# Performance work log

Hardware: AMD Instinct MI355X
Metric: run time of the kernel (lower is better)

## Reference

```python
import jax, jax.numpy as jnp
import numpy as np

NEG_SLOPE = 0.2  # PyG GATConv default leaky_relu slope
EPS = 1e-16     # PyG softmax denominator epsilon


def gat_conv(x, src, dst, edge_attr, W, att_src, att_dst, W_edge, att_edge, bias):
    """Single-head PyG GATConv with edge_dim. x:[N,Fin] -> [N,Fout].
    src/dst already include self-loops; edge_attr matches their length."""
    N = x.shape[0]
    h = x @ W                      # [N, Fout] transformed node features
    a_s = h @ att_src              # [N] per-node source logit contribution
    a_d = h @ att_dst              # [N]
    a_e = (edge_attr @ W_edge) @ att_edge   # [E] edge contribution
    logits = jax.nn.leaky_relu(a_s[src] + a_d[dst] + a_e, NEG_SLOPE)  # [E]
    # segment softmax over destination nodes
    m = jax.ops.segment_max(logits, dst, num_segments=N)    # [N]
    m = jnp.where(jnp.isfinite(m), m, 0.0)
    e = jnp.exp(logits - m[dst])                             # [E]
    denom = jax.ops.segment_sum(e, dst, num_segments=N)      # [N]
    alpha = e / (denom[dst] + EPS)                            # [E]
    # scatter-aggregate weighted messages
    out = jax.ops.segment_sum(alpha[:, None] * h[src], dst, num_segments=N)
    return out + bias


def setup_inputs() -> dict:
    key = jax.random.key(0)
    ks = jax.random.split(key, 16)
    N, E, F_in, H, C, ED = 100000, 1600000, 128, 64, 2, 1
    inp = {
        "x": jax.random.normal(ks[0], (N, F_in), dtype=jnp.float32),
        "edge_index": jax.random.randint(ks[1], (2, E), 0, N, dtype=jnp.int32),
        "edge_attr": jax.random.normal(ks[2], (E, ED), dtype=jnp.float32),
        # layer 1 params (Glorot-ish scale)
        "W1": jax.random.normal(ks[3], (F_in, H), dtype=jnp.float32) * (1.0 / np.sqrt(F_in)),
        "att_src1": jax.random.normal(ks[4], (H,), dtype=jnp.float32) * (1.0 / np.sqrt(H)),
        "att_dst1": jax.random.normal(ks[5], (H,), dtype=jnp.float32) * (1.0 / np.sqrt(H)),
        "W_edge1": jax.random.normal(ks[6], (ED, H), dtype=jnp.float32),
        "att_edge1": jax.random.normal(ks[7], (H,), dtype=jnp.float32) * (1.0 / np.sqrt(H)),
        "bias1": jnp.zeros((H,), dtype=jnp.float32),
        # layer 2 params
        "W2": jax.random.normal(ks[8], (H, C), dtype=jnp.float32) * (1.0 / np.sqrt(H)),
        "att_src2": jax.random.normal(ks[9], (C,), dtype=jnp.float32),
        "att_dst2": jax.random.normal(ks[10], (C,), dtype=jnp.float32),
        "W_edge2": jax.random.normal(ks[11], (ED, C), dtype=jnp.float32),
        "att_edge2": jax.random.normal(ks[12], (C,), dtype=jnp.float32),
        "bias2": jnp.zeros((C,), dtype=jnp.float32),
    }
    return inp


def reference(x, edge_index, edge_attr,
              W1, att_src1, att_dst1, W_edge1, att_edge1, bias1,
              W2, att_src2, att_dst2, W_edge2, att_edge2, bias2):
    N = x.shape[0]
    # PyG GATConv add_self_loops=True, fill_value='mean' for edge_attr
    loop = jnp.arange(N, dtype=edge_index.dtype)
    src = jnp.concatenate([edge_index[0], loop])
    dst = jnp.concatenate([edge_index[1], loop])
    ea_mean = jnp.mean(edge_attr, axis=0, keepdims=True)              # [1, ED]
    ea = jnp.concatenate([edge_attr, jnp.broadcast_to(ea_mean, (N, edge_attr.shape[1]))])

    h = gat_conv(x, src, dst, ea, W1, att_src1, att_dst1, W_edge1, att_edge1, bias1)
    h = jax.nn.relu(h)  # dropout is identity in eval mode
    out = gat_conv(h, src, dst, ea, W2, att_src2, att_dst2, W_edge2, att_edge2, bias2)
    return jax.nn.log_softmax(out, axis=1)
```

## Files before the change

### kernel.cpp

```cpp
#include <hip/hip_runtime.h>
#include <math.h>

#define NEG_SLOPE 0.2f
#define EPSF 1e-16f

constexpr int FIN = 128;
constexpr int H   = 64;
constexpr int C   = 2;
constexpr int BSHIFT = 8;
constexpr int NBUCK_MAX = 1024;
constexpr int CHUNK = 4096;
constexpr int CAP   = 6144;

typedef short v8s __attribute__((ext_vector_type(8)));
typedef float v4f __attribute__((ext_vector_type(4)));
typedef unsigned short u16;

__device__ inline void split_bf16(float v, u16& hi, u16& lo) {
    unsigned u = __float_as_uint(v);
    unsigned r = (u + 0x7FFFu + ((u >> 16) & 1u)) >> 16;
    hi = (u16)r;
    float hf = __uint_as_float(r << 16);
    float l = v - hf;
    unsigned ul = __float_as_uint(l);
    lo = (u16)((ul + 0x7FFFu + ((ul >> 16) & 1u)) >> 16);
}

__device__ inline u16 to_bf16(float v) {
    unsigned u = __float_as_uint(v);
    return (u16)((u + 0x7FFFu + ((u >> 16) & 1u)) >> 16);
}
__device__ inline float blo(int v) { return __uint_as_float((unsigned)v << 16); }
__device__ inline float bhi(int v) { return __uint_as_float((unsigned)v & 0xFFFF0000u); }

__device__ inline int scan1024_excl(int v, int* wtot, int t) {
    int lane = t & 63, w = t >> 6;
    int incl = v;
    #pragma unroll
    for (int o = 1; o < 64; o <<= 1) {
        int u = __shfl_up(incl, o, 64);
        if (lane >= o) incl += u;
    }
    if (lane == 63) wtot[w] = incl;
    __syncthreads();
    int woff = 0;
    for (int i = 0; i < w; i++) woff += wtot[i];
    return woff + incl - v;
}

__global__ __launch_bounds__(1024) void pre_kernel(const float* __restrict__ ea,
                                                   const int* __restrict__ dst, int E,
                                                   float* __restrict__ csum, int* __restrict__ cnt,
                                                   const float* __restrict__ W1,
                                                   u16* __restrict__ Wt_hi, u16* __restrict__ Wt_lo,
                                                   int NBUCK) {
    int c = blockIdx.x, t = threadIdx.x;
    int gid = c * 1024 + t;
    if (gid < FIN * H) {
        int k = gid >> 6, f = gid & 63;
        u16 h, l;
        split_bf16(W1[gid], h, l);
        int idx = ((k >> 3) << 9) + (f << 3) + (k & 7);
        Wt_hi[idx] = h;
        Wt_lo[idx] = l;
    }
    __shared__ int lh[NBUCK_MAX];
    __shared__ float wsum[16];
    lh[t] = 0;
    __syncthreads();
    int base = c * CHUNK;
    int cntE = min(CHUNK, E - base);
    float acc = 0.f;
    for (int i = t; i < cntE; i += 1024) {
        int e = base + i;
        acc += ea[e];
        atomicAdd(&lh[dst[e] >> BSHIFT], 1);
    }
    for (int off = 32; off; off >>= 1) acc += __shfl_down(acc, off, 64);
    int lane = t & 63, wv = t >> 6;
    if (lane == 0) wsum[wv] = acc;
    __syncthreads();
    if (t == 0) {
        float s = 0.f;
        #pragma unroll
        for (int i = 0; i < 16; i++) s += wsum[i];
        csum[c] = s;
    }
    if (t < NBUCK) cnt[(size_t)c * NBUCK + t] = lh[t];
}

__global__ __launch_bounds__(256) void soff_kernel(const int* __restrict__ cnt,
                                                   int NBUCK, int NCHUNK,
                                                   int* __restrict__ bcount, int* __restrict__ poff,
                                                   const float* __restrict__ csum, int E,
                                                   const float* __restrict__ W_edge1,
                                                   const float* __restrict__ att_edge1,
                                                   const float* __restrict__ W_edge2,
                                                   const float* __restrict__ att_edge2,
                                                   float* __restrict__ scal,
                                                   int* __restrict__ rowN) {
    int b = blockIdx.x, t = threadIdx.x;
    int per = (NCHUNK + 255) / 256;
    int v[8];
    int s = 0;
    for (int j = 0; j < per; j++) {
        int c = t * per + j;
        v[j] = (c < NCHUNK) ? cnt[(size_t)c * NBUCK + b] : 0;
        s += v[j];
    }
    __shared__ int red[256];
    __shared__ float ws4[4];
    red[t] = s;
    __syncthreads();
    for (int off = 1; off < 256; off <<= 1) {
        int u = (t >= off) ? red[t - off] : 0;
        __syncthreads();
        red[t] += u;
        __syncthreads();
    }
    int run = red[t] - s;
    for (int j = 0; j < per; j++) {
        int c = t * per + j;
        if (c < NCHUNK) poff[(size_t)b * NCHUNK + c] = run;
        run += v[j];
    }
    if (t == 255) bcount[b] = red[255];
    if (b == 0) {
        float acc = 0.f;
        for (int i = t; i < NCHUNK; i += 256) acc += csum[i];
        for (int off = 32; off; off >>= 1) acc += __shfl_down(acc, off, 64);
        if ((t & 63) == 0) ws4[t >> 6] = acc;
        __syncthreads();
        if (t == 0) {
            float tot = ws4[0] + ws4[1] + ws4[2] + ws4[3];
            float c1 = 0.f;
            for (int i = 0; i < H; i++) c1 += W_edge1[i] * att_edge1[i];
            float c2 = 0.f;
            for (int i = 0; i < C; i++) c2 += W_edge2[i] * att_edge2[i];
            scal[0] = tot / (float)E; scal[1] = c1; scal[2] = c2;
            *rowN = E;
        }
    }
}

__global__ __launch_bounds__(1024) void stage_kernel(
        const int* __restrict__ src, const int* __restrict__ dst, const float* __restrict__ ea,
        int E, const int* __restrict__ cnt, const int* __restrict__ poff,
        const int* __restrict__ bcount,
        int2* __restrict__ staging, int* __restrict__ bbase_out, int NBUCK, int NCHUNK) {
    __shared__ int   bb[NBUCK_MAX];
    __shared__ int   cur[NBUCK_MAX];
    __shared__ int   gofs[NBUCK_MAX];
    __shared__ int2  sbuf[CHUNK];
    __shared__ short sbkt[CHUNK];
    __shared__ int   wt16[16];
    int t = threadIdx.x;
    int c = blockIdx.x;
    int base = c * CHUNK;
    int cntE = min(CHUNK, E - base);
    int bv = (t < NBUCK) ? bcount[t] : 0;
    int bx = scan1024_excl(bv, wt16, t);
    if (t < NBUCK) bb[t] = bx;
    if (c == 0) {
        if (t < NBUCK) bbase_out[t] = bx;
        if (t == 0) bbase_out[NBUCK] = E;
    }
    __syncthreads();
    int h = (t < NBUCK) ? cnt[(size_t)c * NBUCK + t] : 0;
    int p = scan1024_excl(h, wt16, t);
    if (t < NBUCK) {
        if (h) gofs[t] = bb[t] + poff[(size_t)t * NCHUNK + c] - p;
        cur[t] = p;
    }
    __syncthreads();
    for (int i = t; i < cntE; i += 1024) {
        int e = base + i;
        int d = dst[e];
        int b = d >> BSHIFT;
        int slot = atomicAdd(&cur[b], 1);
        sbuf[slot] = make_int2(src[e] | ((d & ((1 << BSHIFT) - 1)) << 20), __float_as_int(ea[e]));
        sbkt[slot] = (short)b;
    }
    __syncthreads();
    for (int j = t; j < cntE; j += 1024)
        staging[gofs[sbkt[j]] + j] = sbuf[j];
}

__global__ __launch_bounds__(256) void gemm1_mfma_kernel(
        const float* __restrict__ x,
        const u16* __restrict__ Wt_hi, const u16* __restrict__ Wt_lo,
        const float* __restrict__ att_src, const float* __restrict__ att_dst,
        u16* __restrict__ h1b, float* __restrict__ a_s, float* __restrict__ a_d, int N) {
    __shared__ u16 WhL[FIN * H];
    __shared__ u16 WlL[FIN * H];
    int t = threadIdx.x;
    int w = t >> 6, lane = t & 63;
    int m = lane & 15, q = lane >> 4;
    int base = blockIdx.x * 128 + w * 32;
    int n0 = base + m;
    int n1 = base + 16 + m;
    bool in0 = n0 < N, in1 = n1 < N;
    const float* xr0 = x + (size_t)n0 * FIN;
    const float* xr1 = x + (size_t)n1 * FIN;

    float4 fh[4], fl4[4];
    {
        const float4* gh = (const float4*)Wt_hi;
        const float4* gl = (const float4*)Wt_lo;
        #pragma unroll
        for (int i = 0; i < 4; i++) {
            fh[i]  = gh[t + i * 256];
            fl4[i] = gl[t + i * 256];
        }
    }
    float4 xa[8], xb[8];
    #pragma unroll
    for (int kt = 0; kt < 4; kt++) {
        if (in0) {
            const float4* p = (const float4*)(xr0 + kt * 32 + q * 8);
            xa[kt * 2] = p[0]; xa[kt * 2 + 1] = p[1];
        } else {
            xa[kt * 2] = make_float4(0.f, 0.f, 0.f, 0.f);
            xa[kt * 2 + 1] = make_float4(0.f, 0.f, 0.f, 0.f);
        }
        if (in1) {
            const float4* p = (const float4*)(xr1 + kt * 32 + q * 8);
            xb[kt * 2] = p[0]; xb[kt * 2 + 1] = p[1];
        } else {
            xb[kt * 2] = make_float4(0.f, 0.f, 0.f, 0.f);
            xb[kt * 2 + 1] = make_float4(0.f, 0.f, 0.f, 0.f);
        }
    }
    {
        float4* sh = (float4*)WhL;
        float4* sl = (float4*)WlL;
        #pragma unroll
        for (int i = 0; i < 4; i++) {
            sh[t + i * 256] = fh[i];
            sl[t + i * 256] = fl4[i];
        }
    }

    v8s ah0[4], al0[4], ah1[4], al1[4];
    #pragma unroll
    for (int kt = 0; kt < 4; kt++) {
        float va[8], vb[8];
        va[0] = xa[kt*2].x; va[1] = xa[kt*2].y; va[2] = xa[kt*2].z; va[3] = xa[kt*2].w;
        va[4] = xa[kt*2+1].x; va[5] = xa[kt*2+1].y; va[6] = xa[kt*2+1].z; va[7] = xa[kt*2+1].w;
        vb[0] = xb[kt*2].x; vb[1] = xb[kt*2].y; vb[2] = xb[kt*2].z; vb[3] = xb[kt*2].w;
        vb[4] = xb[kt*2+1].x; vb[5] = xb[kt*2+1].y; vb[6] = xb[kt*2+1].z; vb[7] = xb[kt*2+1].w;
        #pragma unroll
        for (int j = 0; j < 8; j++) {
            u16 hb, lb;
            split_bf16(va[j], hb, lb);
            ah0[kt][j] = (short)hb; al0[kt][j] = (short)lb;
            split_bf16(vb[j], hb, lb);
            ah1[kt][j] = (short)hb; al1[kt][j] = (short)lb;
        }
    }
    __syncthreads();

    float ps0[4] = {0,0,0,0}, pd0[4] = {0,0,0,0};
    float ps1[4] = {0,0,0,0}, pd1[4] = {0,0,0,0};
    #pragma unroll
    for (int ft = 0; ft < 4; ft++) {
        v4f acc0 = {0.f, 0.f, 0.f, 0.f};
        v4f acc1 = {0.f, 0.f, 0.f, 0.f};
        #pragma unroll
        for (int kt = 0; kt < 4; kt++) {
            int fi = ((kt * 4 + q) << 9) + ((ft * 16 + m) << 3);
            v8s bh = *(const v8s*)(WhL + fi);
            v8s bl = *(const v8s*)(WlL + fi);
            acc0 = __builtin_amdgcn_mfma_f32_16x16x32_bf16(ah0[kt], bh, acc0, 0, 0, 0);
            acc0 = __builtin_amdgcn_mfma_f32_16x16x32_bf16(al0[kt], bh, acc0, 0, 0, 0);
            acc0 = __builtin_amdgcn_mfma_f32_16x16x32_bf16(ah0[kt], bl, acc0, 0, 0, 0);
            acc1 = __builtin_amdgcn_mfma_f32_16x16x32_bf16(ah1[kt], bh, acc1, 0, 0, 0);
            acc1 = __builtin_amdgcn_mfma_f32_16x16x32_bf16(al1[kt], bh, acc1, 0, 0, 0);
            acc1 = __builtin_amdgcn_mfma_f32_16x16x32_bf16(ah1[kt], bl, acc1, 0, 0, 0);
        }
        int f = ft * 16 + m;
        float asf = att_src[f], adf = att_dst[f];
        #pragma unroll
        for (int r = 0; r < 4; r++) {
            int nd0 = base + q * 4 + r;
            int nd1 = base + 16 + q * 4 + r;
            if (nd0 < N) h1b[(size_t)nd0 * H + f] = to_bf16(acc0[r]);
            if (nd1 < N) h1b[(size_t)nd1 * H + f] = to_bf16(acc1[r]);
            ps0[r] += acc0[r] * asf; pd0[r] += acc0[r] * adf;
            ps1[r] += acc1[r] * asf; pd1[r] += acc1[r] * adf;
        }
    }
    #pragma unroll
    for (int msk = 1; msk < 16; msk <<= 1) {
        #pragma unroll
        for (int r = 0; r < 4; r++) {
            ps0[r] += __shfl_xor(ps0[r], msk, 64);
            pd0[r] += __shfl_xor(pd0[r], msk, 64);
            ps1[r] += __shfl_xor(ps1[r], msk, 64);
            pd1[r] += __shfl_xor(pd1[r], msk, 64);
        }
    }
    if (m == 0) {
        #pragma unroll
        for (int r = 0; r < 4; r++) {
            int nd0 = base + q * 4 + r;
            int nd1 = base + 16 + q * 4 + r;
            if (nd0 < N) { a_s[nd0] = ps0[r]; a_d[nd0] = pd0[r]; }
            if (nd1 < N) { a_s[nd1] = ps1[r]; a_d[nd1] = pd1[r]; }
        }
    }
}

__global__ __launch_bounds__(1024) void bfin_kernel(
        const int2* __restrict__ staging, const int* __restrict__ bbase,
        const float* __restrict__ scal,
        const float* __restrict__ a_s1, const float* __restrict__ a_d1,
        int* __restrict__ row, int2* __restrict__ sedge, float* __restrict__ sea2, int N) {
    __shared__ int   nh[256];
    __shared__ int   wt16[16];
    __shared__ int2  ebuf[CAP];
    __shared__ float abuf[CAP];
    int b = blockIdx.x, t = threadIdx.x;
    int beg = bbase[b], end = bbase[b + 1];
    int cnt = end - beg;
    int node0 = b << BSHIFT;
    float c1 = scal[1];
    if (t < 256) nh[t] = 0;
    __syncthreads();
    for (int i = beg + t; i < end; i += 1024)
        atomicAdd(&nh[(unsigned)staging[i].x >> 20], 1);
    __syncthreads();
    int v = (t < 256) ? nh[t] : 0;
    int lane = t & 63, w = t >> 6;
    int incl = v;
    #pragma unroll
    for (int o = 1; o < 64; o <<= 1) {
        int u = __shfl_up(incl, o, 64);
        if (lane >= o) incl += u;
    }
    if (w < 4 && lane == 63) wt16[w] = incl;
    __syncthreads();
    int woff = 0;
    int wl = w < 4 ? w : 4;
    for (int i = 0; i < wl; i++) woff += wt16[i];
    int excl = woff + incl - v;
    int node = node0 + t;
    if (t < 256 && node < N) row[node] = beg + excl;
    bool fast = (cnt <= CAP);
    if (t < 256) nh[t] = fast ? excl : beg + excl;
    __syncthreads();
    for (int i = beg + t; i < end; i += 1024) {
        int2 r = staging[i];
        int dlow = (unsigned)r.x >> 20;
        int sn = r.x & 0xFFFFF;
        float eav = __int_as_float(r.y);
        float lg = a_s1[sn] + a_d1[node0 + dlow] + eav * c1;
        lg = lg > 0.f ? lg : NEG_SLOPE * lg;
        float ex = __expf(lg);
        int pos = atomicAdd(&nh[dlow], 1);
        if (fast) {
            ebuf[pos] = make_int2(sn, __float_as_int(ex));
            abuf[pos] = eav;
        } else {
            sedge[pos] = make_int2(sn, __float_as_int(ex));
            sea2[pos] = eav;
        }
    }
    __syncthreads();
    if (fast) {
        for (int j = t; j < cnt; j += 1024) {
            sedge[beg + j] = ebuf[j];
            sea2[beg + j]  = abuf[j];
        }
    }
}

__device__ inline void accum8(float acc[8], float& den, float xw, int4 hv) {
    den += xw;
    acc[0] += xw * blo(hv.x); acc[1] += xw * bhi(hv.x);
    acc[2] += xw * blo(hv.y); acc[3] += xw * bhi(hv.y);
    acc[4] += xw * blo(hv.z); acc[5] += xw * bhi(hv.z);
    acc[6] += xw * blo(hv.w); acc[7] += xw * bhi(hv.w);
}

__global__ __launch_bounds__(256) void agg1_kernel(
        const int* __restrict__ row, const int2* __restrict__ sedge,
        const float* __restrict__ scal,
        const float* __restrict__ a_s, const float* __restrict__ a_d,
        const u16* __restrict__ h1b,
        const float* __restrict__ bias1, const float* __restrict__ W2,
        const float* __restrict__ att_src2, const float* __restrict__ att_dst2,
        float* __restrict__ h2, float* __restrict__ a_s2, float* __restrict__ a_d2,
        int N) {
    int wv = threadIdx.x >> 6;
    int lane = threadIdx.x & 63;
    int g  = lane >> 3;
    int fl = lane & 7;
    int n = blockIdx.x * 32 + wv * 8 + g;
    if (n >= N) return;
    int beg = row[n], end = row[n + 1];
    float den = 0.f;
    float acc[8] = {0.f, 0.f, 0.f, 0.f, 0.f, 0.f, 0.f, 0.f};
    const u16* hrow = h1b + fl * 8;
    int i = beg;
    for (; i + 8 <= end; i += 8) {
        int2 e[8]; int4 hv[8];
        #pragma unroll
        for (int j = 0; j < 8; j++) e[j] = sedge[i + j];
        #pragma unroll
        for (int j = 0; j < 8; j++) hv[j] = *(const int4*)(hrow + (size_t)e[j].x * H);
        #pragma unroll
        for (int j = 0; j < 8; j++) accum8(acc, den, __int_as_float(e[j].y), hv[j]);
    }
    if (i + 4 <= end) {
        int2 e0 = sedge[i], e1 = sedge[i + 1], e2 = sedge[i + 2], e3 = sedge[i + 3];
        int4 h0 = *(const int4*)(hrow + (size_t)e0.x * H);
        int4 h1v = *(const int4*)(hrow + (size_t)e1.x * H);
        int4 h2v = *(const int4*)(hrow + (size_t)e2.x * H);
        int4 h3v = *(const int4*)(hrow + (size_t)e3.x * H);
        accum8(acc, den, __int_as_float(e0.y), h0);
        accum8(acc, den, __int_as_float(e1.y), h1v);
        accum8(acc, den, __int_as_float(e2.y), h2v);
        accum8(acc, den, __int_as_float(e3.y), h3v);
        i += 4;
    }
    if (i + 2 <= end) {
        int2 e0 = sedge[i], e1 = sedge[i + 1];
        int4 h0 = *(const int4*)(hrow + (size_t)e0.x * H);
        int4 h1v = *(const int4*)(hrow + (size_t)e1.x * H);
        accum8(acc, den, __int_as_float(e0.y), h0);
        accum8(acc, den, __int_as_float(e1.y), h1v);
        i += 2;
    }
    if (i < end) {
        int2 e0 = sedge[i];
        int4 h0 = *(const int4*)(hrow + (size_t)e0.x * H);
        accum8(acc, den, __int_as_float(e0.y), h0);
    }
    {
        float lg = a_s[n] + a_d[n] + scal[0] * scal[1];
        lg = lg > 0.f ? lg : NEG_SLOPE * lg;
        float ex = __expf(lg);
        int4 hs = *(const int4*)(hrow + (size_t)n * H);
        accum8(acc, den, ex, hs);
    }
    float inv = 1.f / (den + EPSF);
    float p0 = 0.f, p1 = 0.f;
    #pragma unroll
    for (int k = 0; k < 8; k++) {
        int f = fl * 8 + k;
        float hr = acc[k] * inv + bias1[f];
        hr = fmaxf(hr, 0.f);
        p0 += hr * W2[f * C + 0];
        p1 += hr * W2[f * C + 1];
    }
    #pragma unroll
    for (int msk = 1; msk < 8; msk <<= 1) {
        p0 += __shfl_xor(p0, msk, 64);
        p1 += __shfl_xor(p1, msk, 64);
    }
    if (fl == 0) {
        h2[(size_t)n * C + 0] = p0;
        h2[(size_t)n * C + 1] = p1;
        a_s2[n] = p0 * att_src2[0] + p1 * att_src2[1];
        a_d2[n] = p0 * att_dst2[0] + p1 * att_dst2[1];
    }
}

__global__ __launch_bounds__(256) void agg2_kernel(
        const int* __restrict__ row, const int2* __restrict__ sedge, const float* __restrict__ sea2,
        const float* __restrict__ scal,
        const float* __restrict__ a_s2, const float* __restrict__ a_d2,
        const float* __restrict__ h2, const float* __restrict__ bias2,
        float* __restrict__ out, int N) {
    int wv = threadIdx.x >> 6;
    int lane = threadIdx.x & 63;
    int g  = lane >> 3;
    int fl = lane & 7;
    int n = blockIdx.x * 32 + wv * 8 + g;
    if (n >= N) return;
    float c2 = scal[2];
    float ad = a_d2[n];
    int beg = row[n], end = row[n + 1];
    float den = 0.f, m0 = 0.f, m1 = 0.f;
    for (int i = beg + fl; i < end; i += 8) {
        int s = sedge[i].x;
        float lg = a_s2[s] + ad + sea2[i] * c2;
        lg = lg > 0.f ? lg : NEG_SLOPE * lg;
        float ex = __expf(lg);
        den += ex;
        m0 += ex * h2[(size_t)s * C + 0];
        m1 += ex * h2[(size_t)s * C + 1];
    }
    if (fl == 0) {
        float lg = a_s2[n] + ad + scal[0] * c2;
        lg = lg > 0.f ? lg : NEG_SLOPE * lg;
        float ex = __expf(lg);
        den += ex;
        m0 += ex * h2[(size_t)n * C + 0];
        m1 += ex * h2[(size_t)n * C + 1];
    }
    #pragma unroll
    for (int msk = 1; msk < 8; msk <<= 1) {
        den += __shfl_xor(den, msk, 64);
        m0  += __shfl_xor(m0, msk, 64);
        m1  += __shfl_xor(m1, msk, 64);
    }
    if (fl == 0) {
        float dn = den + EPSF;
        float o0 = m0 / dn + bias2[0];
        float o1 = m1 / dn + bias2[1];
        float mx = fmaxf(o0, o1);
        float lse = mx + logf(expf(o0 - mx) + expf(o1 - mx));
        out[(size_t)n * C + 0] = o0 - lse;
        out[(size_t)n * C + 1] = o1 - lse;
    }
}

extern "C" void kernel_launch(void* const* d_in, const int* in_sizes, int n_in,
                              void* d_out, int out_size, void* d_ws, size_t ws_size,
                              hipStream_t stream) {
    const float* x        = (const float*)d_in[0];
    const int*   ei       = (const int*)d_in[1];
    const float* ea       = (const float*)d_in[2];
    const float* W1       = (const float*)d_in[3];
    const float* att_src1 = (const float*)d_in[4];
    const float* att_dst1 = (const float*)d_in[5];
    const float* W_edge1  = (const float*)d_in[6];
    const float* att_edge1= (const float*)d_in[7];
    const float* bias1    = (const float*)d_in[8];
    const float* W2       = (const float*)d_in[9];
    const float* att_src2 = (const float*)d_in[10];
    const float* att_dst2 = (const float*)d_in[11];
    const float* W_edge2  = (const float*)d_in[12];
    const float* att_edge2= (const float*)d_in[13];
    const float* bias2    = (const float*)d_in[14];

    const int N  = in_sizes[0] / FIN;
    const int E  = in_sizes[1] / 2;
    const int* srcp = ei;
    const int* dstp = ei + E;
    const int NBUCK  = (N + (1 << BSHIFT) - 1) >> BSHIFT;
    const int NCHUNK = (E + CHUNK - 1) / CHUNK;

    char* wsb = (char*)d_ws;
    size_t off = 0;
    auto alloc = [&](size_t bytes) { void* p = wsb + off; off += (bytes + 255) & ~size_t(255); return p; };
    float* csum   = (float*)alloc((size_t)2048 * 4);
    int*   bcount = (int*)alloc((size_t)NBUCK_MAX * 4);
    int*   bbase  = (int*)alloc((size_t)(NBUCK_MAX + 1) * 4);
    int*   cnt    = (int*)alloc((size_t)NCHUNK * NBUCK * 4);
    int*   poff   = (int*)alloc((size_t)NBUCK * NCHUNK * 4);
    int*   row    = (int*)alloc((size_t)(N + 1) * 4);
    int2*  sedge  = (int2*)alloc((size_t)(E + 8) * 8);
    float* sea2   = (float*)alloc((size_t)E * 4);
    int2*  staging= (int2*)alloc((size_t)E * 8);
    u16*   h1b    = (u16*)alloc((size_t)N * H * 2);
    u16*   Wt_hi  = (u16*)alloc((size_t)FIN * H * 2);
    u16*   Wt_lo  = (u16*)alloc((size_t)FIN * H * 2);
    float* a_s1   = (float*)alloc((size_t)N * 4);
    float* a_d1   = (float*)alloc((size_t)N * 4);
    float* h2     = (float*)alloc((size_t)N * C * 4);
    float* a_s2   = (float*)alloc((size_t)N * 4);
    float* a_d2   = (float*)alloc((size_t)N * 4);
    float* scal   = (float*)alloc(3 * 4);

    pre_kernel<<<NCHUNK, 1024, 0, stream>>>(ea, dstp, E, csum, cnt, W1, Wt_hi, Wt_lo, NBUCK);
    soff_kernel<<<NBUCK, 256, 0, stream>>>(cnt, NBUCK, NCHUNK, bcount, poff,
                                           csum, E, W_edge1, att_edge1, W_edge2, att_edge2,
                                           scal, row + N);
    stage_kernel<<<NCHUNK, 1024, 0, stream>>>(srcp, dstp, ea, E, cnt, poff, bcount,
                                              staging, bbase, NBUCK, NCHUNK);
    gemm1_mfma_kernel<<<(N + 127) / 128, 256, 0, stream>>>(x, Wt_hi, Wt_lo, att_src1, att_dst1,
                                                           h1b, a_s1, a_d1, N);
    bfin_kernel<<<NBUCK, 1024, 0, stream>>>(staging, bbase, scal, a_s1, a_d1, row, sedge, sea2, N);
    agg1_kernel<<<(N + 31) / 32, 256, 0, stream>>>(row, sedge, scal, a_s1, a_d1, h1b,
                                                   bias1, W2, att_src2, att_dst2,
                                                   h2, a_s2, a_d2, N);
    agg2_kernel<<<(N + 31) / 32, 256, 0, stream>>>(row, sedge, sea2, scal, a_s2, a_d2, h2, bias2,
                                                   (float*)d_out, N);
}
```

Baseline: 213.4 us.

## Fuse bucket finalize with layer-1 aggregation using LDS-resident edge lists

Merges bfin and agg1 into one kernel. Each 1024-thread block sorts its 256-node bucket's edges into LDS and aggregates layer-1 messages straight from there, so the sorted edge list is no longer written to and re-read from global memory for layer 1. The sea2 array is dropped by packing the edge attribute into the sedge payload, which agg2 now reads in a single int2 load. The cost is that only 1024 threads per block handle the 256 nodes' gathers, with no 8-way unrolling, and the large LDS footprint limits occupancy during the latency-bound gather phase.

```diff
diff --git a/kernel.cpp b/kernel.cpp
--- a/kernel.cpp
+++ b/kernel.cpp
@@ -311,12 +311,25 @@
     }
 }
 
-__global__ __launch_bounds__(1024) void bfin_kernel(
+__device__ inline void accum8(float acc[8], float& den, float xw, int4 hv) {
+    den += xw;
+    acc[0] += xw * blo(hv.x); acc[1] += xw * bhi(hv.x);
+    acc[2] += xw * blo(hv.y); acc[3] += xw * bhi(hv.y);
+    acc[4] += xw * blo(hv.z); acc[5] += xw * bhi(hv.z);
+    acc[6] += xw * blo(hv.w); acc[7] += xw * bhi(hv.w);
+}
+
+__global__ __launch_bounds__(1024) void bfin_agg1_kernel(
         const int2* __restrict__ staging, const int* __restrict__ bbase,
         const float* __restrict__ scal,
         const float* __restrict__ a_s1, const float* __restrict__ a_d1,
-        int* __restrict__ row, int2* __restrict__ sedge, float* __restrict__ sea2, int N) {
+        const u16* __restrict__ h1b,
+        const float* __restrict__ bias1, const float* __restrict__ W2,
+        const float* __restrict__ att_src2, const float* __restrict__ att_dst2,
+        int* __restrict__ row, int2* __restrict__ sedge,
+        float* __restrict__ h2, float* __restrict__ a_s2, float* __restrict__ a_d2, int N) {
     __shared__ int   nh[256];
+    __shared__ int   bg[256];
     __shared__ int   wt16[16];
     __shared__ int2  ebuf[CAP];
     __shared__ float abuf[CAP];
@@ -344,131 +357,108 @@
     int wl = w < 4 ? w : 4;
     for (int i = 0; i < wl; i++) woff += wt16[i];
     int excl = woff + incl - v;
-    int node = node0 + t;
-    if (t < 256 && node < N) row[node] = beg + excl;
+    if (t < 256 && node0 + t < N) row[node0 + t] = beg + excl;
     bool fast = (cnt <= CAP);
-    if (t < 256) nh[t] = fast ? excl : beg + excl;
+    if (t < 256) {
+        bg[t] = excl;
+        nh[t] = fast ? excl : beg + excl;
+    }
     __syncthreads();
     for (int i = beg + t; i < end; i += 1024) {
         int2 r = staging[i];
         int dlow = (unsigned)r.x >> 20;
         int sn = r.x & 0xFFFFF;
         float eav = __int_as_float(r.y);
-        float lg = a_s1[sn] + a_d1[node0 + dlow] + eav * c1;
-        lg = lg > 0.f ? lg : NEG_SLOPE * lg;
-        float ex = __expf(lg);
         int pos = atomicAdd(&nh[dlow], 1);
         if (fast) {
-            ebuf[pos] = make_int2(sn, __float_as_int(ex));
+            float lg = a_s1[sn] + a_d1[node0 + dlow] + eav * c1;
+            lg = lg > 0.f ? lg : NEG_SLOPE * lg;
+            ebuf[pos] = make_int2(sn, __float_as_int(__expf(lg)));
             abuf[pos] = eav;
         } else {
-            sedge[pos] = make_int2(sn, __float_as_int(ex));
-            sea2[pos] = eav;
+            sedge[pos] = make_int2(sn, __float_as_int(eav));
         }
     }
     __syncthreads();
     if (fast) {
-        for (int j = t; j < cnt; j += 1024) {
-            sedge[beg + j] = ebuf[j];
-            sea2[beg + j]  = abuf[j];
-        }
-    }
-}
-
-__device__ inline void accum8(float acc[8], float& den, float xw, int4 hv) {
-    den += xw;
-    acc[0] += xw * blo(hv.x); acc[1] += xw * bhi(hv.x);
-    acc[2] += xw * blo(hv.y); acc[3] += xw * bhi(hv.y);
-    acc[4] += xw * blo(hv.z); acc[5] += xw * bhi(hv.z);
-    acc[6] += xw * blo(hv.w); acc[7] += xw * bhi(hv.w);
-}
-
-__global__ __launch_bounds__(256) void agg1_kernel(
-        const int* __restrict__ row, const int2* __restrict__ sedge,
-        const float* __restrict__ scal,
-        const float* __restrict__ a_s, const float* __restrict__ a_d,
-        const u16* __restrict__ h1b,
-        const float* __restrict__ bias1, const float* __restrict__ W2,
-        const float* __restrict__ att_src2, const float* __restrict__ att_dst2,
-        float* __restrict__ h2, float* __restrict__ a_s2, float* __restrict__ a_d2,
-        int N) {
-    int wv = threadIdx.x >> 6;
-    int lane = threadIdx.x & 63;
+        for (int j = t; j < cnt; j += 1024)
+            sedge[beg + j] = make_int2(ebuf[j].x, __float_as_int(abuf[j]));
+    }
     int g  = lane >> 3;
     int fl = lane & 7;
-    int n = blockIdx.x * 32 + wv * 8 + g;
-    if (n >= N) return;
-    int beg = row[n], end = row[n + 1];
-    float den = 0.f;
-    float acc[8] = {0.f, 0.f, 0.f, 0.f, 0.f, 0.f, 0.f, 0.f};
+    int wv = t >> 6;
+    float selfc = scal[0] * c1;
     const u16* hrow = h1b + fl * 8;
-    int i = beg;
-    for (; i + 8 <= end; i += 8) {
-        int2 e[8]; int4 hv[8];
-        #pragma unroll
-        for (int j = 0; j < 8; j++) e[j] = sedge[i + j];
-        #pragma unroll
-        for (int j = 0; j < 8; j++) hv[j] = *(const int4*)(hrow + (size_t)e[j].x * H);
-        #pragma unroll
-        for (int j = 0; j < 8; j++) accum8(acc, den, __int_as_float(e[j].y), hv[j]);
-    }
-    if (i + 4 <= end) {
-        int2 e0 = sedge[i], e1 = sedge[i + 1], e2 = sedge[i + 2], e3 = sedge[i + 3];
-        int4 h0 = *(const int4*)(hrow + (size_t)e0.x * H);
-        int4 h1v = *(const int4*)(hrow + (size_t)e1.x * H);
-        int4 h2v = *(const int4*)(hrow + (size_t)e2.x * H);
-        int4 h3v = *(const int4*)(hrow + (size_t)e3.x * H);
-        accum8(acc, den, __int_as_float(e0.y), h0);
-        accum8(acc, den, __int_as_float(e1.y), h1v);
-        accum8(acc, den, __int_as_float(e2.y), h2v);
-        accum8(acc, den, __int_as_float(e3.y), h3v);
-        i += 4;
-    }
-    if (i + 2 <= end) {
-        int2 e0 = sedge[i], e1 = sedge[i + 1];
-        int4 h0 = *(const int4*)(hrow + (size_t)e0.x * H);
-        int4 h1v = *(const int4*)(hrow + (size_t)e1.x * H);
-        accum8(acc, den, __int_as_float(e0.y), h0);
-        accum8(acc, den, __int_as_float(e1.y), h1v);
-        i += 2;
-    }
-    if (i < end) {
-        int2 e0 = sedge[i];
-        int4 h0 = *(const int4*)(hrow + (size_t)e0.x * H);
-        accum8(acc, den, __int_as_float(e0.y), h0);
-    }
-    {
-        float lg = a_s[n] + a_d[n] + scal[0] * scal[1];
-        lg = lg > 0.f ? lg : NEG_SLOPE * lg;
-        float ex = __expf(lg);
-        int4 hs = *(const int4*)(hrow + (size_t)n * H);
-        accum8(acc, den, ex, hs);
-    }
-    float inv = 1.f / (den + EPSF);
-    float p0 = 0.f, p1 = 0.f;
-    #pragma unroll
-    for (int k = 0; k < 8; k++) {
-        int f = fl * 8 + k;
-        float hr = acc[k] * inv + bias1[f];
-        hr = fmaxf(hr, 0.f);
-        p0 += hr * W2[f * C + 0];
-        p1 += hr * W2[f * C + 1];
-    }
-    #pragma unroll
-    for (int msk = 1; msk < 8; msk <<= 1) {
-        p0 += __shfl_xor(p0, msk, 64);
-        p1 += __shfl_xor(p1, msk, 64);
-    }
-    if (fl == 0) {
-        h2[(size_t)n * C + 0] = p0;
-        h2[(size_t)n * C + 1] = p1;
-        a_s2[n] = p0 * att_src2[0] + p1 * att_src2[1];
-        a_d2[n] = p0 * att_dst2[0] + p1 * att_dst2[1];
+    #pragma unroll
+    for (int rr = 0; rr < 2; rr++) {
+        int dlow = rr * 128 + wv * 8 + g;
+        int n = node0 + dlow;
+        if (n >= N) continue;
+        float den = 0.f;
+        float acc[8] = {0.f, 0.f, 0.f, 0.f, 0.f, 0.f, 0.f, 0.f};
+        if (fast) {
+            int i = bg[dlow], i1 = nh[dlow];
+            for (; i + 4 <= i1; i += 4) {
+                int2 e0 = ebuf[i], e1 = ebuf[i + 1], e2 = ebuf[i + 2], e3 = ebuf[i + 3];
+                int4 h0 = *(const int4*)(hrow + (size_t)e0.x * H);
+                int4 h1v = *(const int4*)(hrow + (size_t)e1.x * H);
+                int4 h2v = *(const int4*)(hrow + (size_t)e2.x * H);
+                int4 h3v = *(const int4*)(hrow + (size_t)e3.x * H);
+                accum8(acc, den, __int_as_float(e0.y), h0);
+                accum8(acc, den, __int_as_float(e1.y), h1v);
+                accum8(acc, den, __int_as_float(e2.y), h2v);
+                accum8(acc, den, __int_as_float(e3.y), h3v);
+            }
+            for (; i < i1; i++) {
+                int2 e0 = ebuf[i];
+                int4 h0 = *(const int4*)(hrow + (size_t)e0.x * H);
+                accum8(acc, den, __int_as_float(e0.y), h0);
+            }
+        } else {
+            int i = beg + bg[dlow], i1 = nh[dlow];
+            float adn = a_d1[n];
+            for (; i < i1; i++) {
+                int2 e0 = sedge[i];
+                float lg = a_s1[e0.x] + adn + __int_as_float(e0.y) * c1;
+                lg = lg > 0.f ? lg : NEG_SLOPE * lg;
+                float ex = __expf(lg);
+                int4 h0 = *(const int4*)(hrow + (size_t)e0.x * H);
+                accum8(acc, den, ex, h0);
+            }
+        }
+        {
+            float lg = a_s1[n] + a_d1[n] + selfc;
+            lg = lg > 0.f ? lg : NEG_SLOPE * lg;
+            float ex = __expf(lg);
+            int4 hs = *(const int4*)(hrow + (size_t)n * H);
+            accum8(acc, den, ex, hs);
+        }
+        float inv = 1.f / (den + EPSF);
+        float p0 = 0.f, p1 = 0.f;
+        #pragma unroll
+        for (int k = 0; k < 8; k++) {
+            int f = fl * 8 + k;
+            float hr = acc[k] * inv + bias1[f];
+            hr = fmaxf(hr, 0.f);
+            p0 += hr * W2[f * C + 0];
+            p1 += hr * W2[f * C + 1];
+        }
+        #pragma unroll
+        for (int msk = 1; msk < 8; msk <<= 1) {
+            p0 += __shfl_xor(p0, msk, 64);
+            p1 += __shfl_xor(p1, msk, 64);
+        }
+        if (fl == 0) {
+            h2[(size_t)n * C + 0] = p0;
+            h2[(size_t)n * C + 1] = p1;
+            a_s2[n] = p0 * att_src2[0] + p1 * att_src2[1];
+            a_d2[n] = p0 * att_dst2[0] + p1 * att_dst2[1];
+        }
     }
 }
 
 __global__ __launch_bounds__(256) void agg2_kernel(
-        const int* __restrict__ row, const int2* __restrict__ sedge, const float* __restrict__ sea2,
+        const int* __restrict__ row, const int2* __restrict__ sedge,
         const float* __restrict__ scal,
         const float* __restrict__ a_s2, const float* __restrict__ a_d2,
         const float* __restrict__ h2, const float* __restrict__ bias2,
@@ -484,8 +474,9 @@
     int beg = row[n], end = row[n + 1];
     float den = 0.f, m0 = 0.f, m1 = 0.f;
     for (int i = beg + fl; i < end; i += 8) {
-        int s = sedge[i].x;
-        float lg = a_s2[s] + ad + sea2[i] * c2;
+        int2 e = sedge[i];
+        int s = e.x;
+        float lg = a_s2[s] + ad + __int_as_float(e.y) * c2;
         lg = lg > 0.f ? lg : NEG_SLOPE * lg;
         float ex = __expf(lg);
         den += ex;
@@ -553,7 +544,6 @@
     int*   poff   = (int*)alloc((size_t)NBUCK * NCHUNK * 4);
     int*   row    = (int*)alloc((size_t)(N + 1) * 4);
     int2*  sedge  = (int2*)alloc((size_t)(E + 8) * 8);
-    float* sea2   = (float*)alloc((size_t)E * 4);
     int2*  staging= (int2*)alloc((size_t)E * 8);
     u16*   h1b    = (u16*)alloc((size_t)N * H * 2);
     u16*   Wt_hi  = (u16*)alloc((size_t)FIN * H * 2);
@@ -573,10 +563,9 @@
                                               staging, bbase, NBUCK, NCHUNK);
     gemm1_mfma_kernel<<<(N + 127) / 128, 256, 0, stream>>>(x, Wt_hi, Wt_lo, att_src1, att_dst1,
                                                            h1b, a_s1, a_d1, N);
-    bfin_kernel<<<NBUCK, 1024, 0, stream>>>(staging, bbase, scal, a_s1, a_d1, row, sedge, sea2, N);
-    agg1_kernel<<<(N + 31) / 32, 256, 0, stream>>>(row, sedge, scal, a_s1, a_d1, h1b,
-                                                   bias1, W2, att_src2, att_dst2,
-                                                   h2, a_s2, a_d2, N);
-    agg2_kernel<<<(N + 31) / 32, 256, 0, stream>>>(row, sedge, sea2, scal, a_s2, a_d2, h2, bias2,
+    bfin_agg1_kernel<<<NBUCK, 1024, 0, stream>>>(staging, bbase, scal, a_s1, a_d1, h1b,
+                                                 bias1, W2, att_src2, att_dst2,
+                                                 row, sedge, h2, a_s2, a_d2, N);
+    agg2_kernel<<<(N + 31) / 32, 256, 0, stream>>>(row, sedge, scal, a_s2, a_d2, h2, bias2,
                                                    (float*)d_out, N);
 }
```

Result: faster. 208.6 us (-2.2%).
